# Kernel optimization log

Measured on AMD Instinct MI355X. Metric: run time of the kernel, lower is better.

Reference implementation:

```python
import jax, jax.numpy as jnp
import numpy as np

N, E, IN, H, G = 50000, 800000, 200, 128, 512
L, M = 2, 2
D = H - 1  # Lorentz space dims
EPS = 1e-5


def _l_inner(x, y):
    return -x[..., :1] * y[..., :1] + jnp.sum(x[..., 1:] * y[..., 1:], -1, keepdims=True)


def _proj(x, c):
    s = x[..., 1:]
    t = jnp.sqrt(c + jnp.sum(s * s, -1, keepdims=True))
    return jnp.concatenate([t, s], -1)


def _expmap0(v, c):
    u = v[..., 1:]
    n = jnp.maximum(jnp.linalg.norm(u, axis=-1, keepdims=True), 1e-9)
    sc = jnp.sqrt(c)
    return jnp.concatenate([sc * jnp.cosh(n / sc), sc * jnp.sinh(n / sc) * u / n], -1)


def _logmap0(x, c):
    y = x[..., 1:]
    yn = jnp.maximum(jnp.linalg.norm(y, axis=-1, keepdims=True), 1e-9)
    sc = jnp.sqrt(c)
    d = sc * jnp.arccosh(jnp.maximum(x[..., :1] / sc, 1.0 + EPS))
    return jnp.concatenate([jnp.zeros_like(d), d * y / yn], -1)


def _dist(x, y, c):
    inner = -x[..., 0] * y[..., 0] + jnp.sum(x[..., 1:] * y[..., 1:], -1)
    val = jnp.maximum(-inner / c, 1.0 + EPS)
    return jnp.sqrt(c) * jnp.arccosh(val)


def _hyp_linear(x, w, b, c):
    v = _logmap0(x, c)                      # [n, H], time comp = 0
    os = v[..., 1:] @ w.T + b               # [n, D]
    return _proj(_expmap0(jnp.concatenate([v[..., :1], os], -1), c), c)


def _hyp_act(x, c):
    v = _logmap0(x, c)
    vs = jnp.tanh(v[..., 1:])
    return _expmap0(jnp.concatenate([jnp.zeros_like(v[..., :1]), vs], -1), c)


def _centroid(att, x, src, dst, c):
    # sparse weighted sum: m[i] = sum_{(i,j) in E} att_ij * x[j], then Lorentz normalize
    m = jax.ops.segment_sum(att[:, None] * x[dst], src, num_segments=N)
    denom = jnp.sqrt(jnp.maximum(-_l_inner(m, m), 1e-9))
    return jnp.sqrt(c) * m / denom


def _gin_layer(h, src, dst, aw, ab, eps, mw, mb, c):
    # distance-based attention on linearly transformed features
    hl = _hyp_linear(h, aw, ab, c)
    att = jnp.exp(-_dist(hl[src], hl[dst], c))   # [E]
    agg = _proj(_centroid(att, h, src, dst, c), c)
    hp = _proj(h, c)
    v = _logmap0(agg, c) + (1.0 + eps) * _logmap0(hp, c)
    out = _proj(_expmap0(v, c), c)
    for m in range(M):
        out = _hyp_act(_hyp_linear(out, mw[m], mb[m], c), c)
    return out


def setup_inputs() -> dict:
    key = jax.random.key(0)
    ks = jax.random.split(key, 8)
    x = jax.random.normal(ks[0], (N, IN), jnp.float32) * 0.1
    w_in = jax.random.normal(ks[1], (IN, D), jnp.float32) * (1.0 / np.sqrt(IN))
    att_w = jax.random.normal(ks[2], (L, D, D), jnp.float32) * (1.0 / np.sqrt(D))
    att_b = jnp.zeros((L, D), jnp.float32)
    mlp_w = jax.random.normal(ks[3], (L, M, D, D), jnp.float32) * (1.0 / np.sqrt(D))
    mlp_b = jnp.zeros((L, M, D), jnp.float32)
    eps = jnp.full((L,), 0.1, jnp.float32)
    c = jnp.ones((1,), jnp.float32)
    edge_index = jax.random.randint(ks[4], (2, E), 0, N)
    batch = jnp.sort(jax.random.randint(ks[5], (N,), 0, G))
    return {"x": x, "c": c, "w_in": w_in, "att_w": att_w, "att_b": att_b,
            "eps": eps, "mlp_w": mlp_w, "mlp_b": mlp_b,
            "edge_index": edge_index, "batch": batch}


def reference(x, c, w_in, att_w, att_b, eps, mlp_w, mlp_b, edge_index, batch):
    cc = c[0]
    src, dst = edge_index[0], edge_index[1]
    # Euclidean input proj -> tangent vector at origin -> manifold
    v0 = jnp.concatenate([jnp.zeros((x.shape[0], 1), x.dtype), x @ w_in], -1)
    h = _proj(_expmap0(v0, cc), cc)
    pooled = []
    for l in range(L):
        h = _gin_layer(h, src, dst, att_w[l], att_b[l], eps[l], mlp_w[l], mlp_b[l], cc)
        pooled.append(jax.ops.segment_sum(_logmap0(h, cc), batch, num_segments=G))
    return jnp.concatenate(pooled, -1)  # [G, L*H]
```

## Files before the change

### kernel.cpp

```cpp
#include <hip/hip_runtime.h>
#include <math.h>

#define NN 50000
#define NNP 50048
#define EE 800000
#define IN_F 200
#define DD 127
#define GG 512
#define EPSH 1e-5f

typedef unsigned int u32;
typedef unsigned short u16;
typedef __attribute__((ext_vector_type(8))) short short8;
typedef __attribute__((ext_vector_type(4))) float f32x4;

__device__ __forceinline__ u32 bf16r(float x) {
  u32 u = __float_as_uint(x);
  return (u + 0x7fffu + ((u >> 16) & 1u)) >> 16;
}

__device__ __forceinline__ u32 packhl(float v) {
  u32 hi = bf16r(v);
  float vh = __uint_as_float(hi << 16);
  u32 lo = bf16r(v - vh);
  return hi | (lo << 16);
}

__device__ __forceinline__ float rec(u32 u) {
  return __uint_as_float(u << 16) + __uint_as_float(u & 0xffff0000u);
}

#define WF_TOT (28672 + 6 * 16384)
__global__ void k_prep_wf(const float* __restrict__ att_w, const float* __restrict__ mlp_w,
                          const float* __restrict__ w_in, u16* __restrict__ Wfh,
                          u16* __restrict__ Wfl) {
  for (int idx = blockIdx.x * 256 + threadIdx.x; idx < WF_TOT; idx += gridDim.x * 256) {
    float val;
    if (idx < 28672) {
      int q = idx >> 12, rem = idx & 4095;
      int t = rem >> 9, l = (rem >> 3) & 63, j = rem & 7;
      int k = q * 32 + ((l >> 4) << 3) + j, n = t * 16 + (l & 15);
      val = (k < IN_F && n < DD) ? w_in[k * DD + n] : 0.f;
    } else {
      int rel = idx - 28672;
      int mat = rel >> 14, rem = rel & 16383;
      int q = rem >> 12;
      rem &= 4095;
      int t = rem >> 9, l = (rem >> 3) & 63, j = rem & 7;
      int k = q * 32 + ((l >> 4) << 3) + j, n = t * 16 + (l & 15);
      const float* wsrc = (mat < 2) ? att_w + mat * DD * DD : mlp_w + (mat - 2) * DD * DD;
      val = (k < DD && n < DD) ? wsrc[n * DD + k] : 0.f;
    }
    u32 hi = bf16r(val);
    float vh = __uint_as_float(hi << 16);
    u32 lo = bf16r(val - vh);
    Wfh[idx] = (u16)hi;
    Wfl[idx] = (u16)lo;
  }
}

__global__ void k_count(const int* __restrict__ idx, int n, int* __restrict__ cnt) {
  int i = blockIdx.x * blockDim.x + threadIdx.x;
  if (i < n) atomicAdd(&cnt[idx[i]], 1);
}

__global__ __launch_bounds__(1024) void k_scan_excl(const int* __restrict__ in, int n,
                                                    int* __restrict__ out, int* __restrict__ cur) {
  __shared__ int wbase[16];
  __shared__ int chunk_tot;
  int tid = threadIdx.x;
  int lane = tid & 63;
  int w = tid >> 6;
  int carry = 0;
  for (int base = 0; base < n; base += 1024) {
    int i = base + tid;
    int x = (i < n) ? in[i] : 0;
    int incl = x;
#pragma unroll
    for (int off = 1; off < 64; off <<= 1) {
      int v = __shfl_up(incl, off);
      if (lane >= off) incl += v;
    }
    if (lane == 63) wbase[w] = incl;
    __syncthreads();
    if (w == 0) {
      int t = (lane < 16) ? wbase[lane] : 0;
      int it = t;
#pragma unroll
      for (int off = 1; off < 16; off <<= 1) {
        int v = __shfl_up(it, off);
        if (lane >= off) it += v;
      }
      if (lane < 16) wbase[lane] = it - t;
      if (lane == 15) chunk_tot = it;
    }
    __syncthreads();
    int excl = carry + wbase[w] + (incl - x);
    if (i < n) {
      out[i] = excl;
      if (cur) cur[i] = excl;
    }
    carry += chunk_tot;
    __syncthreads();
  }
  if (tid == 0) out[n] = carry;
}

__global__ void k_scatter(const int* __restrict__ src, const int* __restrict__ dst, int n,
                          int* __restrict__ cursor, int* __restrict__ dst_sorted) {
  int e = blockIdx.x * blockDim.x + threadIdx.x;
  if (e < n) {
    int s = src[e];
    int slot = atomicAdd(&cursor[s], 1);
    dst_sorted[slot] = dst[e];
  }
}

__global__ void k_gptr(const int* __restrict__ batch, int* __restrict__ gptr) {
  int g = blockIdx.x * blockDim.x + threadIdx.x;
  if (g > GG) return;
  int lo = 0, hi = NN;
  while (lo < hi) {
    int mid = (lo + hi) >> 1;
    if (batch[mid] < g) lo = mid + 1; else hi = mid;
  }
  gptr[g] = lo;
}

#define MF_TANH 1
#define MF_T 2
#define MF_P 4

template <int MODE, int AF32>
__global__ __launch_bounds__(256) void k_mgemm(const float* __restrict__ Af,
                                               const u32* __restrict__ A32,
                                               const u16* __restrict__ Wfh,
                                               const u16* __restrict__ Wfl,
                                               const float* __restrict__ bias,
                                               u32* __restrict__ To, u32* __restrict__ Pb,
                                               float* __restrict__ Pt,
                                               const float* __restrict__ cptr, int M) {
  constexpr int NCH = AF32 ? 7 : 4;
  int lane = threadIdx.x & 63, wid = threadIdx.x >> 6;
  int m0 = blockIdx.x * 64 + wid * 16;
  int mld = m0 + (lane & 15);
  int quad = lane >> 4;
  f32x4 acc[8];
#pragma unroll
  for (int t = 0; t < 8; t++) acc[t] = (f32x4){0.f, 0.f, 0.f, 0.f};
#pragma unroll
  for (int q = 0; q < NCH; q++) {
    int k0 = q * 32 + quad * 8;
    union {
      short8 v;
      u32 w[4];
    } ah, al;
    if (AF32) {
      bool ok = (mld < M) && (k0 + 7 < IN_F);
      const float* ap = Af + (size_t)mld * IN_F + k0;
      float4 x0 = ok ? *(const float4*)ap : make_float4(0.f, 0.f, 0.f, 0.f);
      float4 x1 = ok ? *(const float4*)(ap + 4) : make_float4(0.f, 0.f, 0.f, 0.f);
      float xv[8] = {x0.x, x0.y, x0.z, x0.w, x1.x, x1.y, x1.z, x1.w};
#pragma unroll
      for (int p = 0; p < 4; p++) {
        u32 h0 = bf16r(xv[2 * p]), h1 = bf16r(xv[2 * p + 1]);
        float f0 = __uint_as_float(h0 << 16), f1 = __uint_as_float(h1 << 16);
        ah.w[p] = h0 | (h1 << 16);
        al.w[p] = bf16r(xv[2 * p] - f0) | (bf16r(xv[2 * p + 1] - f1) << 16);
      }
    } else {
      const u32* ap = A32 + (size_t)mld * 128 + k0;
      uint4 u0 = *(const uint4*)ap;
      uint4 u1 = *(const uint4*)(ap + 4);
      u32 uu[8] = {u0.x, u0.y, u0.z, u0.w, u1.x, u1.y, u1.z, u1.w};
#pragma unroll
      for (int p = 0; p < 4; p++) {
        ah.w[p] = __builtin_amdgcn_perm(uu[2 * p + 1], uu[2 * p], 0x05040100u);
        al.w[p] = __builtin_amdgcn_perm(uu[2 * p + 1], uu[2 * p], 0x07060302u);
      }
    }
    const u16* bph = Wfh + ((size_t)(q * 8) * 64 + lane) * 8;
    const u16* bpl = Wfl + ((size_t)(q * 8) * 64 + lane) * 8;
#pragma unroll
    for (int t = 0; t < 8; t++) {
      short8 bh = *(const short8*)(bph + t * 512);
      short8 bl = *(const short8*)(bpl + t * 512);
      acc[t] = __builtin_amdgcn_mfma_f32_16x16x32_bf16(ah.v, bh, acc[t], 0, 0, 0);
      acc[t] = __builtin_amdgcn_mfma_f32_16x16x32_bf16(al.v, bh, acc[t], 0, 0, 0);
      acc[t] = __builtin_amdgcn_mfma_f32_16x16x32_bf16(ah.v, bl, acc[t], 0, 0, 0);
    }
  }
  int m = lane & 15;
  float bj[8];
#pragma unroll
  for (int t = 0; t < 8; t++) {
    int col = t * 16 + m;
    bj[t] = (bias != nullptr && col < DD) ? bias[col] : 0.f;
  }
  float cc = 1.f, sc = 1.f;
  if (MODE & MF_P) {
    cc = *cptr;
    sc = sqrtf(cc);
  }
#pragma unroll
  for (int r = 0; r < 4; r++) {
    int rowD = m0 + quad * 4 + r;
    float vs[8];
#pragma unroll
    for (int t = 0; t < 8; t++) {
      float v = acc[t][r] + bj[t];
      if (MODE & MF_TANH) {
        float e = exp2f(v * 2.8853900817779268f);
        v = 1.f - 2.f / (e + 1.f);
      }
      vs[t] = v;
    }
    if ((MODE & MF_T) && rowD < M) {
      u32* to = To + (size_t)rowD * 128 + m;
#pragma unroll
      for (int t = 0; t < 8; t++) to[t * 16] = packhl(vs[t]);
    }
    if (MODE & MF_P) {
      float ps = 0.f;
#pragma unroll
      for (int t = 0; t < 8; t++) ps += vs[t] * vs[t];
#pragma unroll
      for (int off = 1; off < 16; off <<= 1) ps += __shfl_xor(ps, off);
      float nn = fmaxf(sqrtf(ps), 1e-9f);
      float e = expf(nn / sc);
      float f = sc * (e - 1.f / e) * 0.5f / nn;
      float tt = sqrtf(cc + f * f * ps);
      if (rowD < M) {
        u32* pb = Pb + (size_t)rowD * 64 + m;
#pragma unroll
        for (int t = 0; t < 4; t++)
          pb[t * 16] = bf16r(f * vs[t]) | (bf16r(f * vs[t + 4]) << 16);
        if (m == 0) Pt[rowD] = tt;
      }
    }
  }
}

__global__ void k_agg_q(const u32* __restrict__ Hb, const float* __restrict__ ptH,
                        const u32* __restrict__ HLb, const float* __restrict__ ptHL,
                        const u32* __restrict__ T, const int* __restrict__ rowp,
                        const int* __restrict__ dsts, const float* __restrict__ epsp,
                        const float* __restrict__ cptr, u32* __restrict__ Tout, int n) {
  int node = blockIdx.x * 4 + (threadIdx.x >> 6);
  int lane = threadIdx.x & 63;
  if (node >= n) return;
  int p = lane & 15;
  int q = lane >> 4;
  float c = *cptr, sc = sqrtf(c), rcpc = 1.f / c;
  float eps = *epsp;
  uint4 a4 = *(const uint4*)(HLb + (size_t)node * 64 + p * 4);
  float alo[4], ahi[4];
  {
    u32 aw[4] = {a4.x, a4.y, a4.z, a4.w};
#pragma unroll
    for (int j = 0; j < 4; j++) {
      alo[j] = __uint_as_float(aw[j] << 16);
      ahi[j] = __uint_as_float(aw[j] & 0xffff0000u);
    }
  }
  float pts = ptHL[node];
  int e0 = rowp[node], e1 = rowp[node + 1];
  int iters = (e1 - e0 + 3) >> 2;
  float m[8] = {0.f, 0.f, 0.f, 0.f, 0.f, 0.f, 0.f, 0.f};
  float mt = 0.f;
#pragma unroll 2
  for (int it = 0; it < iters; it++) {
    int e = e0 + it * 4 + q;
    bool ve = e < e1;
    int ei = ve ? e : e0;
    int d = dsts[ei];
    uint4 b4 = *(const uint4*)(HLb + (size_t)d * 64 + p * 4);
    float ptd = ptHL[d];
    float pth = ptH[d];
    u32 bw[4] = {b4.x, b4.y, b4.z, b4.w};
    float dot = 0.f;
#pragma unroll
    for (int j = 0; j < 4; j++) {
      dot = fmaf(alo[j], __uint_as_float(bw[j] << 16), dot);
      dot = fmaf(ahi[j], __uint_as_float(bw[j] & 0xffff0000u), dot);
    }
#pragma unroll
    for (int off = 1; off < 16; off <<= 1) dot += __shfl_xor(dot, off);
    float valv = fmaxf((pts * ptd - dot) * rcpc, 1.f + EPSH);
    float w = valv + sqrtf(fmaf(valv, valv, -1.f));
    float att = exp2f(-sc * __log2f(w));
    att = ve ? att : 0.f;
    uint4 h4 = *(const uint4*)(Hb + (size_t)d * 64 + p * 4);
    u32 hw[4] = {h4.x, h4.y, h4.z, h4.w};
#pragma unroll
    for (int j = 0; j < 4; j++) {
      m[j] = fmaf(att, __uint_as_float(hw[j] << 16), m[j]);
      m[4 + j] = fmaf(att, __uint_as_float(hw[j] & 0xffff0000u), m[4 + j]);
    }
    mt = fmaf(att, pth, mt);
  }
#pragma unroll
  for (int j = 0; j < 8; j++) {
    m[j] += __shfl_xor(m[j], 16);
    m[j] += __shfl_xor(m[j], 32);
  }
  mt += __shfl_xor(mt, 16);
  mt += __shfl_xor(mt, 32);
  float lp = 0.f;
#pragma unroll
  for (int j = 0; j < 8; j++) lp = fmaf(m[j], m[j], lp);
#pragma unroll
  for (int off = 1; off < 16; off <<= 1) lp += __shfl_xor(lp, off);
  float lsq = lp;
  float neg_inner = mt * mt - lsq;
  float denom = sqrtf(fmaxf(neg_inner, 1e-9f));
  float r = sc / denom;
  float ssq = r * r * lsq;
  float agg0 = sqrtf(c + ssq);
  float ynA = fmaxf(sqrtf(ssq), 1e-9f);
  float v2 = fmaxf(agg0 / sc, 1.f + EPSH);
  float dA = sc * 0.69314718056f * __log2f(v2 + sqrtf(v2 * v2 - 1.f));
  float sca = dA * r / ynA;
  uint4 t0 = *(const uint4*)(T + (size_t)node * 128 + p * 4);
  uint4 t1 = *(const uint4*)(T + (size_t)node * 128 + 64 + p * 4);
  u32 tw0[4] = {t0.x, t0.y, t0.z, t0.w};
  u32 tw1[4] = {t1.x, t1.y, t1.z, t1.w};
  float oe = 1.f + eps;
  uint4 o0, o1;
  u32* po0 = (u32*)&o0;
  u32* po1 = (u32*)&o1;
#pragma unroll
  for (int j = 0; j < 4; j++) {
    po0[j] = packhl(fmaf(sca, m[j], oe * rec(tw0[j])));
    po1[j] = packhl(fmaf(sca, m[4 + j], oe * rec(tw1[j])));
  }
  if (q == 0) {
    *(uint4*)(Tout + (size_t)node * 128 + p * 4) = o0;
    *(uint4*)(Tout + (size_t)node * 128 + 64 + p * 4) = o1;
  }
}

__global__ void k_pool(const u32* __restrict__ U, const int* __restrict__ gptr,
                       float* __restrict__ out, int layer) {
  int g = blockIdx.x;
  int c = threadIdx.x;
  int s = gptr[g], e = gptr[g + 1];
  float acc = 0.f;
  if (c > 0) {
    const u32* up = U + (c - 1);
    int i = s;
    float a0 = 0.f, a1 = 0.f, a2 = 0.f, a3 = 0.f;
    for (; i + 3 < e; i += 4) {
      a0 += rec(up[(size_t)i * 128]);
      a1 += rec(up[(size_t)(i + 1) * 128]);
      a2 += rec(up[(size_t)(i + 2) * 128]);
      a3 += rec(up[(size_t)(i + 3) * 128]);
    }
    for (; i < e; i++) a0 += rec(up[(size_t)i * 128]);
    acc = (a0 + a1) + (a2 + a3);
  }
  out[(size_t)g * 256 + layer * 128 + c] = acc;
}

extern "C" void kernel_launch(void* const* d_in, const int* in_sizes, int n_in, void* d_out,
                              int out_size, void* d_ws, size_t ws_size, hipStream_t stream) {
  const float* x = (const float*)d_in[0];
  const float* cptr = (const float*)d_in[1];
  const float* w_in = (const float*)d_in[2];
  const float* att_w = (const float*)d_in[3];
  const float* att_b = (const float*)d_in[4];
  const float* epsv = (const float*)d_in[5];
  const float* mlp_w = (const float*)d_in[6];
  const float* mlp_b = (const float*)d_in[7];
  const int* ei = (const int*)d_in[8];
  const int* batch = (const int*)d_in[9];
  const int* srcp = ei;
  const int* dstp = ei + EE;
  float* out = (float*)d_out;

  u32* ws = (u32*)d_ws;
  u16* Wfh = (u16*)ws;
  u16* Wfl = Wfh + WF_TOT;
  int* deg = (int*)(ws + 126976);
  int* rowp = deg + NN;
  int* cursor = rowp + NN + 1;
  int* gptr = cursor + NN;
  int* dsts = gptr + GG + 1;
  float* ptH = (float*)(dsts + EE);
  float* ptHL = ptH + NNP;
  size_t o2 = (size_t)((u32*)(ptHL + NNP) - ws);
  o2 = (o2 + 3) & ~(size_t)3;
  u32* Hb = ws + o2;
  u32* HLb = Hb + (size_t)NNP * 64;
  u32* A32 = HLb + (size_t)NNP * 64;
  u32* B32 = A32 + (size_t)NNP * 128;

  const int EW = 12500;
  const int GEMMG = (NN + 63) / 64;

  hipMemsetAsync(deg, 0, NN * sizeof(int), stream);
  k_prep_wf<<<64, 256, 0, stream>>>(att_w, mlp_w, w_in, Wfh, Wfl);
  k_count<<<(EE + 255) / 256, 256, 0, stream>>>(srcp, EE, deg);
  k_gptr<<<3, 256, 0, stream>>>(batch, gptr);
  k_scan_excl<<<1, 1024, 0, stream>>>(deg, NN, rowp, cursor);
  k_scatter<<<(EE + 255) / 256, 256, 0, stream>>>(srcp, dstp, EE, cursor, dsts);

#define WH(m) (Wfh + 28672 + (m) * 16384)
#define WL(m) (Wfl + 28672 + (m) * 16384)

  k_mgemm<MF_T | MF_P, 1><<<GEMMG, 256, 0, stream>>>(x, nullptr, Wfh, Wfl, nullptr, A32, Hb, ptH, cptr, NN);

  k_mgemm<MF_P, 0><<<GEMMG, 256, 0, stream>>>(nullptr, A32, WH(0), WL(0), att_b, nullptr, HLb, ptHL, cptr, NN);
  k_agg_q<<<EW, 256, 0, stream>>>(Hb, ptH, HLb, ptHL, A32, rowp, dsts, epsv + 0, cptr, B32, NN);
  k_mgemm<MF_TANH | MF_T, 0><<<GEMMG, 256, 0, stream>>>(nullptr, B32, WH(2), WL(2), mlp_b + 0 * DD, B32, nullptr, nullptr, cptr, NN);
  k_mgemm<MF_TANH | MF_T | MF_P, 0><<<GEMMG, 256, 0, stream>>>(nullptr, B32, WH(3), WL(3), mlp_b + 1 * DD, A32, Hb, ptH, cptr, NN);
  k_pool<<<GG, 128, 0, stream>>>(A32, gptr, out, 0);

  k_mgemm<MF_P, 0><<<GEMMG, 256, 0, stream>>>(nullptr, A32, WH(1), WL(1), att_b + DD, nullptr, HLb, ptHL, cptr, NN);
  k_agg_q<<<EW, 256, 0, stream>>>(Hb, ptH, HLb, ptHL, A32, rowp, dsts, epsv + 1, cptr, B32, NN);
  k_mgemm<MF_TANH | MF_T, 0><<<GEMMG, 256, 0, stream>>>(nullptr, B32, WH(4), WL(4), mlp_b + 2 * DD, B32, nullptr, nullptr, cptr, NN);
  k_mgemm<MF_TANH | MF_T, 0><<<GEMMG, 256, 0, stream>>>(nullptr, B32, WH(5), WL(5), mlp_b + 3 * DD, B32, nullptr, nullptr, cptr, NN);
  k_pool<<<GG, 128, 0, stream>>>(B32, gptr, out, 1);
}
```

Measured before the change: 587.6 us.

## Fuse MLP GEMM pairs via LDS, interleave H/HL rows, vectorize scan

After: 547.0 us. 1.07x faster.

```diff
diff --git a/kernel.cpp b/kernel.cpp
--- a/kernel.cpp
+++ b/kernel.cpp
@@ -72,14 +72,17 @@
   int lane = tid & 63;
   int w = tid >> 6;
   int carry = 0;
-  for (int base = 0; base < n; base += 1024) {
-    int i = base + tid;
-    int x = (i < n) ? in[i] : 0;
+  for (int base = 0; base < n; base += 4096) {
+    int i0 = base + tid * 4;
+    int v[4];
+#pragma unroll
+    for (int j = 0; j < 4; j++) v[j] = (i0 + j < n) ? in[i0 + j] : 0;
+    int x = v[0] + v[1] + v[2] + v[3];
     int incl = x;
 #pragma unroll
     for (int off = 1; off < 64; off <<= 1) {
-      int v = __shfl_up(incl, off);
-      if (lane >= off) incl += v;
+      int t = __shfl_up(incl, off);
+      if (lane >= off) incl += t;
     }
     if (lane == 63) wbase[w] = incl;
     __syncthreads();
@@ -88,17 +91,21 @@
       int it = t;
 #pragma unroll
       for (int off = 1; off < 16; off <<= 1) {
-        int v = __shfl_up(it, off);
-        if (lane >= off) it += v;
+        int v2 = __shfl_up(it, off);
+        if (lane >= off) it += v2;
       }
       if (lane < 16) wbase[lane] = it - t;
       if (lane == 15) chunk_tot = it;
     }
     __syncthreads();
-    int excl = carry + wbase[w] + (incl - x);
-    if (i < n) {
-      out[i] = excl;
-      if (cur) cur[i] = excl;
+    int run = carry + wbase[w] + (incl - x);
+#pragma unroll
+    for (int j = 0; j < 4; j++) {
+      if (i0 + j < n) {
+        out[i0 + j] = run;
+        if (cur) cur[i0 + j] = run;
+      }
+      run += v[j];
     }
     carry += chunk_tot;
     __syncthreads();
@@ -130,6 +137,71 @@
 #define MF_TANH 1
 #define MF_T 2
 #define MF_P 4
+
+__device__ __forceinline__ void afrag_from_f32(const float* xv, u32* ahw, u32* alw) {
+#pragma unroll
+  for (int p = 0; p < 4; p++) {
+    u32 h0 = bf16r(xv[2 * p]), h1 = bf16r(xv[2 * p + 1]);
+    float f0 = __uint_as_float(h0 << 16), f1 = __uint_as_float(h1 << 16);
+    ahw[p] = h0 | (h1 << 16);
+    alw[p] = bf16r(xv[2 * p] - f0) | (bf16r(xv[2 * p + 1] - f1) << 16);
+  }
+}
+
+template <int MODE>
+__device__ __forceinline__ void epilogue(f32x4* acc, const float* __restrict__ bias,
+                                         u32* __restrict__ To, u32* __restrict__ Pb,
+                                         float* __restrict__ Pt, const float* __restrict__ cptr,
+                                         int m0, int quad, int ml, int M) {
+  float bj[8];
+#pragma unroll
+  for (int t = 0; t < 8; t++) {
+    int col = t * 16 + ml;
+    bj[t] = (bias != nullptr && col < DD) ? bias[col] : 0.f;
+  }
+  float cc = 1.f, sc = 1.f;
+  if (MODE & MF_P) {
+    cc = *cptr;
+    sc = sqrtf(cc);
+  }
+#pragma unroll
+  for (int r = 0; r < 4; r++) {
+    int rowD = m0 + quad * 4 + r;
+    float vs[8];
+#pragma unroll
+    for (int t = 0; t < 8; t++) {
+      float v = acc[t][r] + bj[t];
+      if (MODE & MF_TANH) {
+        float e = exp2f(v * 2.8853900817779268f);
+        v = 1.f - 2.f / (e + 1.f);
+      }
+      vs[t] = v;
+    }
+    if ((MODE & MF_T) && rowD < M) {
+      u32* to = To + (size_t)rowD * 128 + ml;
+#pragma unroll
+      for (int t = 0; t < 8; t++) to[t * 16] = packhl(vs[t]);
+    }
+    if (MODE & MF_P) {
+      float ps = 0.f;
+#pragma unroll
+      for (int t = 0; t < 8; t++) ps += vs[t] * vs[t];
+#pragma unroll
+      for (int off = 1; off < 16; off <<= 1) ps += __shfl_xor(ps, off);
+      float nn = fmaxf(sqrtf(ps), 1e-9f);
+      float e = expf(nn / sc);
+      float f = sc * (e - 1.f / e) * 0.5f / nn;
+      float tt = sqrtf(cc + f * f * ps);
+      if (rowD < M) {
+        u32* pb = Pb + (size_t)rowD * 128 + ml;
+#pragma unroll
+        for (int t = 0; t < 4; t++)
+          pb[t * 16] = bf16r(f * vs[t]) | (bf16r(f * vs[t + 4]) << 16);
+        if (ml == 0) Pt[rowD * 2] = tt;
+      }
+    }
+  }
+}
 
 template <int MODE, int AF32>
 __global__ __launch_bounds__(256) void k_mgemm(const float* __restrict__ Af,
@@ -143,7 +215,8 @@
   constexpr int NCH = AF32 ? 7 : 4;
   int lane = threadIdx.x & 63, wid = threadIdx.x >> 6;
   int m0 = blockIdx.x * 64 + wid * 16;
-  int mld = m0 + (lane & 15);
+  int ml = lane & 15;
+  int mld = m0 + ml;
   int quad = lane >> 4;
   f32x4 acc[8];
 #pragma unroll
@@ -161,13 +234,7 @@
       float4 x0 = ok ? *(const float4*)ap : make_float4(0.f, 0.f, 0.f, 0.f);
       float4 x1 = ok ? *(const float4*)(ap + 4) : make_float4(0.f, 0.f, 0.f, 0.f);
       float xv[8] = {x0.x, x0.y, x0.z, x0.w, x1.x, x1.y, x1.z, x1.w};
-#pragma unroll
-      for (int p = 0; p < 4; p++) {
-        u32 h0 = bf16r(xv[2 * p]), h1 = bf16r(xv[2 * p + 1]);
-        float f0 = __uint_as_float(h0 << 16), f1 = __uint_as_float(h1 << 16);
-        ah.w[p] = h0 | (h1 << 16);
-        al.w[p] = bf16r(xv[2 * p] - f0) | (bf16r(xv[2 * p + 1] - f1) << 16);
-      }
+      afrag_from_f32(xv, ah.w, al.w);
     } else {
       const u32* ap = A32 + (size_t)mld * 128 + k0;
       uint4 u0 = *(const uint4*)ap;
@@ -190,59 +257,103 @@
       acc[t] = __builtin_amdgcn_mfma_f32_16x16x32_bf16(ah.v, bl, acc[t], 0, 0, 0);
     }
   }
-  int m = lane & 15;
-  float bj[8];
-#pragma unroll
-  for (int t = 0; t < 8; t++) {
-    int col = t * 16 + m;
-    bj[t] = (bias != nullptr && col < DD) ? bias[col] : 0.f;
-  }
-  float cc = 1.f, sc = 1.f;
-  if (MODE & MF_P) {
-    cc = *cptr;
-    sc = sqrtf(cc);
-  }
-#pragma unroll
-  for (int r = 0; r < 4; r++) {
-    int rowD = m0 + quad * 4 + r;
-    float vs[8];
+  epilogue<MODE>(acc, bias, To, Pb, Pt, cptr, m0, quad, ml, M);
+}
+
+template <int MODE>
+__global__ __launch_bounds__(256) void k_mgemm_mlp(const u32* __restrict__ A32,
+                                                   const u16* __restrict__ Wha,
+                                                   const u16* __restrict__ Wla,
+                                                   const float* __restrict__ ba,
+                                                   const u16* __restrict__ Whb,
+                                                   const u16* __restrict__ Wlb,
+                                                   const float* __restrict__ bb,
+                                                   u32* __restrict__ To, u32* __restrict__ Pb,
+                                                   float* __restrict__ Pt,
+                                                   const float* __restrict__ cptr, int M) {
+  __shared__ float tile[4][16][129];
+  int lane = threadIdx.x & 63, wid = threadIdx.x >> 6;
+  int m0 = blockIdx.x * 64 + wid * 16;
+  int ml = lane & 15;
+  int mld = m0 + ml;
+  int quad = lane >> 4;
+  f32x4 acc[8];
+#pragma unroll
+  for (int t = 0; t < 8; t++) acc[t] = (f32x4){0.f, 0.f, 0.f, 0.f};
+#pragma unroll
+  for (int q = 0; q < 4; q++) {
+    int k0 = q * 32 + quad * 8;
+    union {
+      short8 v;
+      u32 w[4];
+    } ah, al;
+    const u32* ap = A32 + (size_t)mld * 128 + k0;
+    uint4 u0 = *(const uint4*)ap;
+    uint4 u1 = *(const uint4*)(ap + 4);
+    u32 uu[8] = {u0.x, u0.y, u0.z, u0.w, u1.x, u1.y, u1.z, u1.w};
+#pragma unroll
+    for (int p = 0; p < 4; p++) {
+      ah.w[p] = __builtin_amdgcn_perm(uu[2 * p + 1], uu[2 * p], 0x05040100u);
+      al.w[p] = __builtin_amdgcn_perm(uu[2 * p + 1], uu[2 * p], 0x07060302u);
+    }
+    const u16* bph = Wha + ((size_t)(q * 8) * 64 + lane) * 8;
+    const u16* bpl = Wla + ((size_t)(q * 8) * 64 + lane) * 8;
 #pragma unroll
     for (int t = 0; t < 8; t++) {
-      float v = acc[t][r] + bj[t];
-      if (MODE & MF_TANH) {
+      short8 bh = *(const short8*)(bph + t * 512);
+      short8 bl = *(const short8*)(bpl + t * 512);
+      acc[t] = __builtin_amdgcn_mfma_f32_16x16x32_bf16(ah.v, bh, acc[t], 0, 0, 0);
+      acc[t] = __builtin_amdgcn_mfma_f32_16x16x32_bf16(al.v, bh, acc[t], 0, 0, 0);
+      acc[t] = __builtin_amdgcn_mfma_f32_16x16x32_bf16(ah.v, bl, acc[t], 0, 0, 0);
+    }
+  }
+  {
+    float bj[8];
+#pragma unroll
+    for (int t = 0; t < 8; t++) {
+      int col = t * 16 + ml;
+      bj[t] = (col < DD) ? ba[col] : 0.f;
+    }
+#pragma unroll
+    for (int r = 0; r < 4; r++) {
+#pragma unroll
+      for (int t = 0; t < 8; t++) {
+        float v = acc[t][r] + bj[t];
         float e = exp2f(v * 2.8853900817779268f);
         v = 1.f - 2.f / (e + 1.f);
+        tile[wid][quad * 4 + r][t * 16 + ml] = v;
       }
-      vs[t] = v;
-    }
-    if ((MODE & MF_T) && rowD < M) {
-      u32* to = To + (size_t)rowD * 128 + m;
-#pragma unroll
-      for (int t = 0; t < 8; t++) to[t * 16] = packhl(vs[t]);
-    }
-    if (MODE & MF_P) {
-      float ps = 0.f;
-#pragma unroll
-      for (int t = 0; t < 8; t++) ps += vs[t] * vs[t];
-#pragma unroll
-      for (int off = 1; off < 16; off <<= 1) ps += __shfl_xor(ps, off);
-      float nn = fmaxf(sqrtf(ps), 1e-9f);
-      float e = expf(nn / sc);
-      float f = sc * (e - 1.f / e) * 0.5f / nn;
-      float tt = sqrtf(cc + f * f * ps);
-      if (rowD < M) {
-        u32* pb = Pb + (size_t)rowD * 64 + m;
-#pragma unroll
-        for (int t = 0; t < 4; t++)
-          pb[t * 16] = bf16r(f * vs[t]) | (bf16r(f * vs[t + 4]) << 16);
-        if (m == 0) Pt[rowD] = tt;
-      }
-    }
-  }
-}
-
-__global__ void k_agg_q(const u32* __restrict__ Hb, const float* __restrict__ ptH,
-                        const u32* __restrict__ HLb, const float* __restrict__ ptHL,
+    }
+  }
+  __syncthreads();
+#pragma unroll
+  for (int t = 0; t < 8; t++) acc[t] = (f32x4){0.f, 0.f, 0.f, 0.f};
+#pragma unroll
+  for (int q = 0; q < 4; q++) {
+    int k0 = q * 32 + quad * 8;
+    float xv[8];
+#pragma unroll
+    for (int j = 0; j < 8; j++) xv[j] = tile[wid][ml][k0 + j];
+    union {
+      short8 v;
+      u32 w[4];
+    } ah, al;
+    afrag_from_f32(xv, ah.w, al.w);
+    const u16* bph = Whb + ((size_t)(q * 8) * 64 + lane) * 8;
+    const u16* bpl = Wlb + ((size_t)(q * 8) * 64 + lane) * 8;
+#pragma unroll
+    for (int t = 0; t < 8; t++) {
+      short8 bh = *(const short8*)(bph + t * 512);
+      short8 bl = *(const short8*)(bpl + t * 512);
+      acc[t] = __builtin_amdgcn_mfma_f32_16x16x32_bf16(ah.v, bh, acc[t], 0, 0, 0);
+      acc[t] = __builtin_amdgcn_mfma_f32_16x16x32_bf16(al.v, bh, acc[t], 0, 0, 0);
+      acc[t] = __builtin_amdgcn_mfma_f32_16x16x32_bf16(ah.v, bl, acc[t], 0, 0, 0);
+    }
+  }
+  epilogue<MODE>(acc, bb, To, Pb, Pt, cptr, m0, quad, ml, M);
+}
+
+__global__ void k_agg_q(const u32* __restrict__ HHb, const float2* __restrict__ ptHH,
                         const u32* __restrict__ T, const int* __restrict__ rowp,
                         const int* __restrict__ dsts, const float* __restrict__ epsp,
                         const float* __restrict__ cptr, u32* __restrict__ Tout, int n) {
@@ -253,7 +364,7 @@
   int q = lane >> 4;
   float c = *cptr, sc = sqrtf(c), rcpc = 1.f / c;
   float eps = *epsp;
-  uint4 a4 = *(const uint4*)(HLb + (size_t)node * 64 + p * 4);
+  uint4 a4 = *(const uint4*)(HHb + (size_t)node * 128 + p * 4);
   float alo[4], ahi[4];
   {
     u32 aw[4] = {a4.x, a4.y, a4.z, a4.w};
@@ -263,7 +374,7 @@
       ahi[j] = __uint_as_float(aw[j] & 0xffff0000u);
     }
   }
-  float pts = ptHL[node];
+  float pts = ptHH[node].x;
   int e0 = rowp[node], e1 = rowp[node + 1];
   int iters = (e1 - e0 + 3) >> 2;
   float m[8] = {0.f, 0.f, 0.f, 0.f, 0.f, 0.f, 0.f, 0.f};
@@ -274,9 +385,10 @@
     bool ve = e < e1;
     int ei = ve ? e : e0;
     int d = dsts[ei];
-    uint4 b4 = *(const uint4*)(HLb + (size_t)d * 64 + p * 4);
-    float ptd = ptHL[d];
-    float pth = ptH[d];
+    const u32* rb = HHb + (size_t)d * 128 + p * 4;
+    uint4 b4 = *(const uint4*)rb;
+    uint4 h4 = *(const uint4*)(rb + 64);
+    float2 pp = ptHH[d];
     u32 bw[4] = {b4.x, b4.y, b4.z, b4.w};
     float dot = 0.f;
 #pragma unroll
@@ -286,18 +398,17 @@
     }
 #pragma unroll
     for (int off = 1; off < 16; off <<= 1) dot += __shfl_xor(dot, off);
-    float valv = fmaxf((pts * ptd - dot) * rcpc, 1.f + EPSH);
+    float valv = fmaxf((pts * pp.x - dot) * rcpc, 1.f + EPSH);
     float w = valv + sqrtf(fmaf(valv, valv, -1.f));
     float att = exp2f(-sc * __log2f(w));
     att = ve ? att : 0.f;
-    uint4 h4 = *(const uint4*)(Hb + (size_t)d * 64 + p * 4);
     u32 hw[4] = {h4.x, h4.y, h4.z, h4.w};
 #pragma unroll
     for (int j = 0; j < 4; j++) {
       m[j] = fmaf(att, __uint_as_float(hw[j] << 16), m[j]);
       m[4 + j] = fmaf(att, __uint_as_float(hw[j] & 0xffff0000u), m[4 + j]);
     }
-    mt = fmaf(att, pth, mt);
+    mt = fmaf(att, pp.y, mt);
   }
 #pragma unroll
   for (int j = 0; j < 8; j++) {
@@ -386,13 +497,11 @@
   int* cursor = rowp + NN + 1;
   int* gptr = cursor + NN;
   int* dsts = gptr + GG + 1;
-  float* ptH = (float*)(dsts + EE);
-  float* ptHL = ptH + NNP;
-  size_t o2 = (size_t)((u32*)(ptHL + NNP) - ws);
-  o2 = (o2 + 3) & ~(size_t)3;
-  u32* Hb = ws + o2;
-  u32* HLb = Hb + (size_t)NNP * 64;
-  u32* A32 = HLb + (size_t)NNP * 64;
+  size_t o1 = (size_t)((u32*)(dsts + EE) - ws);
+  o1 = (o1 + 3) & ~(size_t)3;
+  float2* ptHH = (float2*)(ws + o1);
+  u32* HHb = ws + o1 + 2 * NNP;
+  u32* A32 = HHb + (size_t)NNP * 128;
   u32* B32 = A32 + (size_t)NNP * 128;
 
   const int EW = 12500;
@@ -407,18 +516,24 @@
 
 #define WH(m) (Wfh + 28672 + (m) * 16384)
 #define WL(m) (Wfl + 28672 + (m) * 16384)
-
-  k_mgemm<MF_T | MF_P, 1><<<GEMMG, 256, 0, stream>>>(x, nullptr, Wfh, Wfl, nullptr, A32, Hb, ptH, cptr, NN);
-
-  k_mgemm<MF_P, 0><<<GEMMG, 256, 0, stream>>>(nullptr, A32, WH(0), WL(0), att_b, nullptr, HLb, ptHL, cptr, NN);
-  k_agg_q<<<EW, 256, 0, stream>>>(Hb, ptH, HLb, ptHL, A32, rowp, dsts, epsv + 0, cptr, B32, NN);
-  k_mgemm<MF_TANH | MF_T, 0><<<GEMMG, 256, 0, stream>>>(nullptr, B32, WH(2), WL(2), mlp_b + 0 * DD, B32, nullptr, nullptr, cptr, NN);
-  k_mgemm<MF_TANH | MF_T | MF_P, 0><<<GEMMG, 256, 0, stream>>>(nullptr, B32, WH(3), WL(3), mlp_b + 1 * DD, A32, Hb, ptH, cptr, NN);
+  float* ptX = (float*)ptHH;
+
+  k_mgemm<MF_T | MF_P, 1><<<GEMMG, 256, 0, stream>>>(x, nullptr, Wfh, Wfl, nullptr, A32,
+                                                     HHb + 64, ptX + 1, cptr, NN);
+
+  k_mgemm<MF_P, 0><<<GEMMG, 256, 0, stream>>>(nullptr, A32, WH(0), WL(0), att_b, nullptr, HHb,
+                                              ptX, cptr, NN);
+  k_agg_q<<<EW, 256, 0, stream>>>(HHb, ptHH, A32, rowp, dsts, epsv + 0, cptr, B32, NN);
+  k_mgemm_mlp<MF_TANH | MF_T | MF_P><<<GEMMG, 256, 0, stream>>>(
+      B32, WH(2), WL(2), mlp_b + 0 * DD, WH(3), WL(3), mlp_b + 1 * DD, A32, HHb + 64, ptX + 1,
+      cptr, NN);
   k_pool<<<GG, 128, 0, stream>>>(A32, gptr, out, 0);
 
-  k_mgemm<MF_P, 0><<<GEMMG, 256, 0, stream>>>(nullptr, A32, WH(1), WL(1), att_b + DD, nullptr, HLb, ptHL, cptr, NN);
-  k_agg_q<<<EW, 256, 0, stream>>>(Hb, ptH, HLb, ptHL, A32, rowp, dsts, epsv + 1, cptr, B32, NN);
-  k_mgemm<MF_TANH | MF_T, 0><<<GEMMG, 256, 0, stream>>>(nullptr, B32, WH(4), WL(4), mlp_b + 2 * DD, B32, nullptr, nullptr, cptr, NN);
-  k_mgemm<MF_TANH | MF_T, 0><<<GEMMG, 256, 0, stream>>>(nullptr, B32, WH(5), WL(5), mlp_b + 3 * DD, B32, nullptr, nullptr, cptr, NN);
+  k_mgemm<MF_P, 0><<<GEMMG, 256, 0, stream>>>(nullptr, A32, WH(1), WL(1), att_b + DD, nullptr,
+                                              HHb, ptX, cptr, NN);
+  k_agg_q<<<EW, 256, 0, stream>>>(HHb, ptHH, A32, rowp, dsts, epsv + 1, cptr, B32, NN);
+  k_mgemm_mlp<MF_TANH | MF_T><<<GEMMG, 256, 0, stream>>>(B32, WH(4), WL(4), mlp_b + 2 * DD,
+                                                         WH(5), WL(5), mlp_b + 3 * DD, B32,
+                                                         nullptr, nullptr, cptr, NN);
   k_pool<<<GG, 128, 0, stream>>>(B32, gptr, out, 1);
 }
```
